# Performance work log

Hardware: AMD Instinct MI355X
Metric: run time of the kernel (lower is better)

## Reference

```python
import jax, jax.numpy as jnp
import numpy as np

N_HEADS = 16
D_MODEL = 1024
D_HEAD = D_MODEL // N_HEADS


def setup_inputs() -> dict:
    key = jax.random.key(0)
    k1, k2, k3 = jax.random.split(key, 3)
    b, t, d = 2, 2048, D_MODEL
    x = jax.random.normal(k1, (b, t, d), dtype=jnp.float32)
    # Linear weights stored as [in, out] so y = x @ W (equivalent to torch's x @ W.T)
    w_qkv = jax.random.normal(k2, (d, 3 * d), dtype=jnp.float32) * (1.0 / np.sqrt(d))
    w_out = jax.random.normal(k3, (d, d), dtype=jnp.float32) * (1.0 / np.sqrt(d))
    return {"x": x, "w_qkv": w_qkv, "w_out": w_out}


def reference(x, w_qkv, w_out):
    b, t, d = x.shape
    h, dh = N_HEADS, D_HEAD
    qkv = x @ w_qkv                                   # (b, t, 3d)
    q, k, v = jnp.split(qkv, 3, axis=-1)
    # (b, h, t, dh)
    q = q.reshape(b, t, h, dh).transpose(0, 2, 1, 3)
    k = k.reshape(b, t, h, dh).transpose(0, 2, 1, 3)
    v = v.reshape(b, t, h, dh).transpose(0, 2, 1, 3)
    scale = 1.0 / np.sqrt(dh).astype(np.float32)
    att = jnp.einsum('bhqd,bhkd->bhqk', q, k) * scale  # (b, h, t, t)
    causal = jnp.tril(jnp.ones((t, t), dtype=bool))
    att = jnp.where(causal, att, -jnp.inf)
    att = jax.nn.softmax(att, axis=-1)
    y = jnp.einsum('bhqk,bhkd->bhqd', att, v)          # (b, h, t, dh)
    y = y.transpose(0, 2, 1, 3).reshape(b, t, d)
    return y @ w_out
```

## Files before the change

### kernel.cpp

```cpp
#include <hip/hip_runtime.h>
#include <hip/hip_bf16.h>
#include <stdint.h>

typedef __bf16 bf16x8 __attribute__((ext_vector_type(8)));
typedef float  f32x4  __attribute__((ext_vector_type(4)));

#define B_   2
#define T_   2048
#define H_   16
#define DH_  64
#define DM_  1024
#define BH_  (B_*H_)
#define M_   (B_*T_)

#define QSCALE 0.18033688f
#define FIXED_M 8.0f

static __device__ __forceinline__ void gload_lds16(const void* g, void* lds) {
  __builtin_amdgcn_global_load_lds(
      (const __attribute__((address_space(1))) void*)(uintptr_t)g,
      (__attribute__((address_space(3))) void*)(uint32_t)(uintptr_t)lds,
      16, 0, 0);
}

__global__ void k_cvt_bf16(const float* __restrict__ in, __hip_bfloat16* __restrict__ out, int n4) {
  int i = blockIdx.x * blockDim.x + threadIdx.x;
  if (i < n4) {
    float4 v = reinterpret_cast<const float4*>(in)[i];
    alignas(8) __hip_bfloat16 t[4] = {__float2bfloat16(v.x), __float2bfloat16(v.y),
                                      __float2bfloat16(v.z), __float2bfloat16(v.w)};
    reinterpret_cast<uint2*>(out)[i] = *reinterpret_cast<const uint2*>(t);
  }
}

__global__ void k_cvtT(const float* __restrict__ in, __hip_bfloat16* __restrict__ out, int K, int N) {
  __shared__ float tile[32][33];
  int n0 = blockIdx.x * 32, k0 = blockIdx.y * 32;
  int tid = threadIdx.x;
  int kl = tid >> 3, n4 = (tid & 7) * 4;
  float4 v = *reinterpret_cast<const float4*>(in + (size_t)(k0 + kl) * N + n0 + n4);
  tile[kl][n4 + 0] = v.x; tile[kl][n4 + 1] = v.y; tile[kl][n4 + 2] = v.z; tile[kl][n4 + 3] = v.w;
  __syncthreads();
  int nl = tid >> 3, k4 = (tid & 7) * 4;
  alignas(8) __hip_bfloat16 t[4];
  #pragma unroll
  for (int j = 0; j < 4; ++j) t[j] = __float2bfloat16(tile[k4 + j][nl]);
  *reinterpret_cast<uint2*>(out + (size_t)(n0 + nl) * K + k0 + k4) = *reinterpret_cast<const uint2*>(t);
}

template<int BM, int BN, int FM, int FN>
static __device__ __forceinline__ void gemm_core(
    const __hip_bfloat16* __restrict__ A, const __hip_bfloat16* __restrict__ BT,
    int K, int brow, int bcol, __hip_bfloat16* As, __hip_bfloat16* Bs, f32x4 acc[FM][FN]) {
  constexpr int WGN = BN / (16 * FN);
  const int tid = threadIdx.x, wave = tid >> 6, lane = tid & 63;
  const int wr = wave / WGN, wc = wave % WGN;
  const int llo = lane & 15, lhi = lane >> 4;
  for (int k0 = 0; k0 < K; k0 += 32) {
    #pragma unroll
    for (int c = wave; c < BM / 16; c += 4)
      gload_lds16(A + (size_t)(brow + c * 16 + (lane >> 2)) * K + k0 + (lane & 3) * 8,
                  As + c * 16 * 32);
    #pragma unroll
    for (int c = wave; c < BN / 16; c += 4)
      gload_lds16(BT + (size_t)(bcol + c * 16 + (lane >> 2)) * K + k0 + (lane & 3) * 8,
                  Bs + c * 16 * 32);
    __syncthreads();
    bf16x8 a[FM], b[FN];
    #pragma unroll
    for (int i = 0; i < FM; ++i)
      a[i] = *reinterpret_cast<const bf16x8*>(As + (wr * FM * 16 + i * 16 + llo) * 32 + lhi * 8);
    #pragma unroll
    for (int j = 0; j < FN; ++j)
      b[j] = *reinterpret_cast<const bf16x8*>(Bs + (wc * FN * 16 + j * 16 + llo) * 32 + lhi * 8);
    #pragma unroll
    for (int i = 0; i < FM; ++i)
      #pragma unroll
      for (int j = 0; j < FN; ++j)
        acc[i][j] = __builtin_amdgcn_mfma_f32_16x16x32_bf16(a[i], b[j], acc[i][j], 0, 0, 0);
    __syncthreads();
  }
}

__global__ __launch_bounds__(256) void k_gemm_qkv(
    const __hip_bfloat16* __restrict__ A, const __hip_bfloat16* __restrict__ BT,
    __hip_bfloat16* __restrict__ q_ws, __hip_bfloat16* __restrict__ k_ws,
    __hip_bfloat16* __restrict__ vT) {
  alignas(16) __shared__ __hip_bfloat16 As[128 * 32];
  alignas(16) __shared__ __hip_bfloat16 Bs[128 * 32];
  f32x4 acc[4][4] = {};
  const int brow = blockIdx.y * 128, bcol = blockIdx.x * 128;
  gemm_core<128, 128, 4, 4>(A, BT, DM_, brow, bcol, As, Bs, acc);
  const int tid = threadIdx.x, wave = tid >> 6, lane = tid & 63;
  const int wr = wave >> 1, wc = wave & 1;
  const int llo = lane & 15, lhi = lane >> 4;
  #pragma unroll
  for (int i = 0; i < 4; ++i) {
    const int tbase = brow + wr * 64 + i * 16 + lhi * 4;
    const int b = tbase >> 11, t = tbase & 2047;
    #pragma unroll
    for (int j = 0; j < 4; ++j) {
      int n = bcol + wc * 64 + j * 16 + llo;
      int part = n >> 10, rem = n & 1023, hh = rem >> 6, dh = rem & 63;
      if (part == 2) {
        alignas(8) __hip_bfloat16 tv[4];
        #pragma unroll
        for (int r = 0; r < 4; ++r) tv[r] = __float2bfloat16(acc[i][j][r]);
        *reinterpret_cast<uint2*>(
            vT + (((size_t)(b * H_ + hh)) * DH_ + dh) * T_ + t) =
            *reinterpret_cast<const uint2*>(tv);
      } else {
        float sc = (part == 0) ? QSCALE : 1.0f;
        __hip_bfloat16* dst = (part == 0) ? q_ws : k_ws;
        #pragma unroll
        for (int r = 0; r < 4; ++r)
          dst[(((size_t)(b * H_ + hh)) * T_ + t + r) * DH_ + dh] =
              __float2bfloat16(acc[i][j][r] * sc);
      }
    }
  }
}

__global__ __launch_bounds__(256) void k_gemm_out(
    const __hip_bfloat16* __restrict__ A, const __hip_bfloat16* __restrict__ BT,
    float* __restrict__ C) {
  alignas(16) __shared__ __hip_bfloat16 As[128 * 32];
  alignas(16) __shared__ __hip_bfloat16 Bs[64 * 32];
  f32x4 acc[4][2] = {};
  const int brow = blockIdx.y * 128, bcol = blockIdx.x * 64;
  gemm_core<128, 64, 4, 2>(A, BT, DM_, brow, bcol, As, Bs, acc);
  const int tid = threadIdx.x, wave = tid >> 6, lane = tid & 63;
  const int wr = wave >> 1, wc = wave & 1;
  const int llo = lane & 15, lhi = lane >> 4;
  #pragma unroll
  for (int i = 0; i < 4; ++i)
    #pragma unroll
    for (int j = 0; j < 2; ++j) {
      int n = bcol + wc * 32 + j * 16 + llo;
      #pragma unroll
      for (int r = 0; r < 4; ++r) {
        int m = brow + wr * 64 + i * 16 + lhi * 4 + r;
        C[(size_t)m * DM_ + n] = acc[i][j][r];
      }
    }
}

__global__ __launch_bounds__(512) void k_attn(
    const __hip_bfloat16* __restrict__ Q, const __hip_bfloat16* __restrict__ Kk,
    const __hip_bfloat16* __restrict__ VT, __hip_bfloat16* __restrict__ Y) {
  alignas(16) __shared__ __hip_bfloat16 Ks[2][64 * 64];
  alignas(16) __shared__ __hip_bfloat16 Vs[2][64 * 64];
  alignas(16) __shared__ __hip_bfloat16 Ps[8][16 * 64];
  const int bh = blockIdx.y;
  const int p  = blockIdx.x;
  const int tid = threadIdx.x, wave = tid >> 6, lane = tid & 63;
  const int llo = lane & 15, lhi = lane >> 4;
  const int qt   = (wave < 4) ? (31 - p) : p;
  const int myNt = qt + 1;
  const int ntA  = 32 - p;
  const int q0 = qt * 64;
  const int qbase = q0 + (wave & 3) * 16;

  const __hip_bfloat16* kb = Kk + (size_t)bh * T_ * DH_;
  const __hip_bfloat16* vb = VT + (size_t)bh * DH_ * T_;

  const int srow = lane >> 3;
  const int schunk = (lane & 7) ^ srow;
  const int rb = wave * 8;

  bf16x8 aq[2];
  #pragma unroll
  for (int k0 = 0; k0 < 2; ++k0)
    aq[k0] = *reinterpret_cast<const bf16x8*>(
        Q + ((size_t)bh * T_ + qbase + llo) * DH_ + k0 * 32 + lhi * 8);

  float lrow[4] = {0.f, 0.f, 0.f, 0.f};
  f32x4 o[4] = {};

  gload_lds16(kb + (size_t)(rb + srow) * DH_ + schunk * 8, &Ks[0][rb * 64]);
  gload_lds16(vb + (size_t)(rb + srow) * T_ + schunk * 8, &Vs[0][rb * 64]);
  __syncthreads();

  for (int it = 0; it < ntA; ++it) {
    const int cur = it & 1;
    if (it + 1 < ntA) {
      const int tn = (it + 1) * 64;
      gload_lds16(kb + (size_t)(tn + rb + srow) * DH_ + schunk * 8, &Ks[cur ^ 1][rb * 64]);
      gload_lds16(vb + (size_t)(rb + srow) * T_ + tn + schunk * 8, &Vs[cur ^ 1][rb * 64]);
    }
    if (it < myNt) {
      const __hip_bfloat16* ksb = Ks[cur];
      const __hip_bfloat16* vsb = Vs[cur];

      f32x4 s[4];
      __builtin_amdgcn_s_setprio(1);
      #pragma unroll
      for (int jn = 0; jn < 4; ++jn) {
        const __hip_bfloat16* krow = ksb + (jn * 16 + llo) * 64;
        bf16x8 b0 = *reinterpret_cast<const bf16x8*>(krow + ((lhi ^ (llo & 7)) << 3));
        bf16x8 b1 = *reinterpret_cast<const bf16x8*>(krow + (((4 + lhi) ^ (llo & 7)) << 3));
        f32x4 z = {};
        z = __builtin_amdgcn_mfma_f32_16x16x32_bf16(aq[0], b0, z, 0, 0, 0);
        z = __builtin_amdgcn_mfma_f32_16x16x32_bf16(aq[1], b1, z, 0, 0, 0);
        s[jn] = z;
      }
      __builtin_amdgcn_s_setprio(0);
      if (it == myNt - 1) {
        #pragma unroll
        for (int jn = 0; jn < 4; ++jn)
          #pragma unroll
          for (int r = 0; r < 4; ++r) {
            int qrow = qbase + lhi * 4 + r;
            int tcol = q0 + jn * 16 + llo;
            if (tcol > qrow) s[jn][r] = -INFINITY;
          }
      }
      #pragma unroll
      for (int jn = 0; jn < 4; ++jn)
        #pragma unroll
        for (int r = 0; r < 4; ++r) {
          float pv = __builtin_amdgcn_exp2f(s[jn][r] - FIXED_M);
          lrow[r] += pv;
          int row = lhi * 4 + r, col = jn * 16 + llo;
          Ps[wave][row * 64 + (col ^ ((row & 7) << 3))] = __float2bfloat16(pv);
        }
      bf16x8 ap0 = *reinterpret_cast<const bf16x8*>(
          &Ps[wave][llo * 64 + ((lhi ^ (llo & 7)) << 3)]);
      bf16x8 ap1 = *reinterpret_cast<const bf16x8*>(
          &Ps[wave][llo * 64 + (((4 + lhi) ^ (llo & 7)) << 3)]);
      __builtin_amdgcn_s_setprio(1);
      #pragma unroll
      for (int jd = 0; jd < 4; ++jd) {
        const __hip_bfloat16* vrow = vsb + (jd * 16 + llo) * 64;
        bf16x8 b0 = *reinterpret_cast<const bf16x8*>(vrow + ((lhi ^ (llo & 7)) << 3));
        bf16x8 b1 = *reinterpret_cast<const bf16x8*>(vrow + (((4 + lhi) ^ (llo & 7)) << 3));
        o[jd] = __builtin_amdgcn_mfma_f32_16x16x32_bf16(ap0, b0, o[jd], 0, 0, 0);
        o[jd] = __builtin_amdgcn_mfma_f32_16x16x32_bf16(ap1, b1, o[jd], 0, 0, 0);
      }
      __builtin_amdgcn_s_setprio(0);
    }
    __syncthreads();
  }

  float lr[4];
  #pragma unroll
  for (int r = 0; r < 4; ++r) {
    float ps = lrow[r];
    #pragma unroll
    for (int d = 1; d < 16; d <<= 1) ps += __shfl_xor(ps, d);
    lr[r] = ps;
  }
  const int b = bh >> 4, h = bh & 15;
  #pragma unroll
  for (int jd = 0; jd < 4; ++jd)
    #pragma unroll
    for (int r = 0; r < 4; ++r) {
      int trow = qbase + lhi * 4 + r;
      int col = h * 64 + jd * 16 + llo;
      Y[((size_t)(b * T_ + trow)) * DM_ + col] = __float2bfloat16(o[jd][r] / lr[r]);
    }
}

extern "C" void kernel_launch(void* const* d_in, const int* in_sizes, int n_in,
                              void* d_out, int out_size, void* d_ws, size_t ws_size,
                              hipStream_t stream) {
  const float* x     = (const float*)d_in[0];
  const float* w_qkv = (const float*)d_in[1];
  const float* w_out = (const float*)d_in[2];
  float* out = (float*)d_out;
  char* ws = (char*)d_ws;

  size_t off = 0;
  __hip_bfloat16* xb    = (__hip_bfloat16*)(ws + off); off += (size_t)M_ * DM_ * 2;
  __hip_bfloat16* wqkvT = (__hip_bfloat16*)(ws + off); off += (size_t)3 * DM_ * DM_ * 2;
  __hip_bfloat16* woutT = (__hip_bfloat16*)(ws + off); off += (size_t)DM_ * DM_ * 2;
  __hip_bfloat16* q_ws  = (__hip_bfloat16*)(ws + off); off += (size_t)M_ * DM_ * 2;
  __hip_bfloat16* k_ws  = (__hip_bfloat16*)(ws + off); off += (size_t)M_ * DM_ * 2;
  __hip_bfloat16* vT    = (__hip_bfloat16*)(ws + off); off += (size_t)M_ * DM_ * 2;
  __hip_bfloat16* y_ws  = (__hip_bfloat16*)(ws + off); off += (size_t)M_ * DM_ * 2;
  (void)ws_size; (void)in_sizes; (void)n_in; (void)out_size;

  k_cvt_bf16<<<(M_ * DM_ / 4 + 255) / 256, 256, 0, stream>>>(x, xb, M_ * DM_ / 4);
  k_cvtT<<<dim3(3 * DM_ / 32, DM_ / 32), 256, 0, stream>>>(w_qkv, wqkvT, DM_, 3 * DM_);
  k_cvtT<<<dim3(DM_ / 32, DM_ / 32), 256, 0, stream>>>(w_out, woutT, DM_, DM_);

  k_gemm_qkv<<<dim3(3 * DM_ / 128, M_ / 128), 256, 0, stream>>>(xb, wqkvT, q_ws, k_ws, vT);

  k_attn<<<dim3(T_ / 128, BH_), 512, 0, stream>>>(q_ws, k_ws, vT, y_ws);

  k_gemm_out<<<dim3(DM_ / 64, M_ / 128), 256, 0, stream>>>(y_ws, woutT, out);
}
```

Baseline: 115.8 us.

## Split-K balance attention tiles between wave groups with per-group K/V staging

The attention block previously had one wave group own the long query tile and the other the short one, so the short group sat idle for many iterations. Now each group stages its own K/V tiles into separate double buffers, and the short group helps the long tile by handling the back half of its key range. The helper's partial output and row sums are merged through LDS at the end, which works because the kernel uses a fixed softmax max. The loop count drops to 17 iterations, at the cost of doubled K/V shared memory, extra registers for the helper accumulators, and a final reduction step.

New measurement: 113.7 us. About the same (-1.8%).

```diff
diff --git a/kernel.cpp b/kernel.cpp
--- a/kernel.cpp
+++ b/kernel.cpp
@@ -145,119 +145,172 @@
     }
 }
 
-__global__ __launch_bounds__(512) void k_attn(
+static __device__ __forceinline__ void attn_tile(
+    const __hip_bfloat16* ksb, const __hip_bfloat16* vsb, __hip_bfloat16* PsW,
+    const bf16x8* aq, int llo, int lhi, int qbase, int tile, bool do_mask,
+    f32x4* o, float* lrow) {
+  f32x4 s[4];
+  __builtin_amdgcn_s_setprio(1);
+  #pragma unroll
+  for (int jn = 0; jn < 4; ++jn) {
+    const __hip_bfloat16* krow = ksb + (jn * 16 + llo) * 64;
+    bf16x8 b0 = *reinterpret_cast<const bf16x8*>(krow + ((lhi ^ (llo & 7)) << 3));
+    bf16x8 b1 = *reinterpret_cast<const bf16x8*>(krow + (((4 + lhi) ^ (llo & 7)) << 3));
+    f32x4 z = {};
+    z = __builtin_amdgcn_mfma_f32_16x16x32_bf16(aq[0], b0, z, 0, 0, 0);
+    z = __builtin_amdgcn_mfma_f32_16x16x32_bf16(aq[1], b1, z, 0, 0, 0);
+    s[jn] = z;
+  }
+  __builtin_amdgcn_s_setprio(0);
+  if (do_mask) {
+    #pragma unroll
+    for (int jn = 0; jn < 4; ++jn)
+      #pragma unroll
+      for (int r = 0; r < 4; ++r) {
+        int qrow = qbase + lhi * 4 + r;
+        int tcol = tile * 64 + jn * 16 + llo;
+        if (tcol > qrow) s[jn][r] = -INFINITY;
+      }
+  }
+  #pragma unroll
+  for (int jn = 0; jn < 4; ++jn)
+    #pragma unroll
+    for (int r = 0; r < 4; ++r) {
+      float pv = __builtin_amdgcn_exp2f(s[jn][r] - FIXED_M);
+      lrow[r] += pv;
+      int row = lhi * 4 + r, col = jn * 16 + llo;
+      PsW[row * 64 + (col ^ ((row & 7) << 3))] = __float2bfloat16(pv);
+    }
+  bf16x8 ap0 = *reinterpret_cast<const bf16x8*>(&PsW[llo * 64 + ((lhi ^ (llo & 7)) << 3)]);
+  bf16x8 ap1 = *reinterpret_cast<const bf16x8*>(&PsW[llo * 64 + (((4 + lhi) ^ (llo & 7)) << 3)]);
+  __builtin_amdgcn_s_setprio(1);
+  #pragma unroll
+  for (int jd = 0; jd < 4; ++jd) {
+    const __hip_bfloat16* vrow = vsb + (jd * 16 + llo) * 64;
+    bf16x8 b0 = *reinterpret_cast<const bf16x8*>(vrow + ((lhi ^ (llo & 7)) << 3));
+    bf16x8 b1 = *reinterpret_cast<const bf16x8*>(vrow + (((4 + lhi) ^ (llo & 7)) << 3));
+    o[jd] = __builtin_amdgcn_mfma_f32_16x16x32_bf16(ap0, b0, o[jd], 0, 0, 0);
+    o[jd] = __builtin_amdgcn_mfma_f32_16x16x32_bf16(ap1, b1, o[jd], 0, 0, 0);
+  }
+  __builtin_amdgcn_s_setprio(0);
+}
+
+__global__ __launch_bounds__(512, 4) void k_attn(
     const __hip_bfloat16* __restrict__ Q, const __hip_bfloat16* __restrict__ Kk,
     const __hip_bfloat16* __restrict__ VT, __hip_bfloat16* __restrict__ Y) {
-  alignas(16) __shared__ __hip_bfloat16 Ks[2][64 * 64];
-  alignas(16) __shared__ __hip_bfloat16 Vs[2][64 * 64];
+  alignas(16) __shared__ __hip_bfloat16 Ks[4][64 * 64];
+  alignas(16) __shared__ __hip_bfloat16 Vs[4][64 * 64];
   alignas(16) __shared__ __hip_bfloat16 Ps[8][16 * 64];
   const int bh = blockIdx.y;
   const int p  = blockIdx.x;
   const int tid = threadIdx.x, wave = tid >> 6, lane = tid & 63;
   const int llo = lane & 15, lhi = lane >> 4;
-  const int qt   = (wave < 4) ? (31 - p) : p;
-  const int myNt = qt + 1;
-  const int ntA  = 32 - p;
-  const int q0 = qt * 64;
-  const int qbase = q0 + (wave & 3) * 16;
+  const int group = wave >> 2, ws = wave & 3;
+  const int qtA = 31 - p, qtB = p;
+  const int qt_own = group ? qtB : qtA;
+  const int qb_own  = qt_own * 64 + ws * 16;
+  const int qb_help = qtA * 64 + ws * 16;
 
   const __hip_bfloat16* kb = Kk + (size_t)bh * T_ * DH_;
   const __hip_bfloat16* vb = VT + (size_t)bh * DH_ * T_;
 
   const int srow = lane >> 3;
   const int schunk = (lane & 7) ^ srow;
-  const int rb = wave * 8;
-
-  bf16x8 aq[2];
-  #pragma unroll
-  for (int k0 = 0; k0 < 2; ++k0)
-    aq[k0] = *reinterpret_cast<const bf16x8*>(
-        Q + ((size_t)bh * T_ + qbase + llo) * DH_ + k0 * 32 + lhi * 8);
-
-  float lrow[4] = {0.f, 0.f, 0.f, 0.f};
-  f32x4 o[4] = {};
-
-  gload_lds16(kb + (size_t)(rb + srow) * DH_ + schunk * 8, &Ks[0][rb * 64]);
-  gload_lds16(vb + (size_t)(rb + srow) * T_ + schunk * 8, &Vs[0][rb * 64]);
+  const int rbase = ws * 16;
+
+  auto seq = [&](int j) -> int {
+    if (group == 0) return (j <= 16) ? j : -1;
+    if (j <= p) return j;
+    if (j <= 15) return 32 - j;
+    return -1;
+  };
+  auto stage = [&](int tile, int slot) {
+    gload_lds16(kb + (size_t)(tile * 64 + rbase + srow) * DH_ + schunk * 8,
+                &Ks[slot][rbase * 64]);
+    gload_lds16(kb + (size_t)(tile * 64 + rbase + 8 + srow) * DH_ + schunk * 8,
+                &Ks[slot][(rbase + 8) * 64]);
+    gload_lds16(vb + (size_t)(rbase + srow) * T_ + tile * 64 + schunk * 8,
+                &Vs[slot][rbase * 64]);
+    gload_lds16(vb + (size_t)(rbase + 8 + srow) * T_ + tile * 64 + schunk * 8,
+                &Vs[slot][(rbase + 8) * 64]);
+  };
+
+  bf16x8 aq_own[2], aq_help[2];
+  #pragma unroll
+  for (int k0 = 0; k0 < 2; ++k0) {
+    aq_own[k0] = *reinterpret_cast<const bf16x8*>(
+        Q + ((size_t)bh * T_ + qb_own + llo) * DH_ + k0 * 32 + lhi * 8);
+    aq_help[k0] = *reinterpret_cast<const bf16x8*>(
+        Q + ((size_t)bh * T_ + qb_help + llo) * DH_ + k0 * 32 + lhi * 8);
+  }
+
+  float l_own[4] = {0.f, 0.f, 0.f, 0.f}, l_help[4] = {0.f, 0.f, 0.f, 0.f};
+  f32x4 o_own[4] = {}, o_help[4] = {};
+
+  stage(0, group * 2);
   __syncthreads();
 
-  for (int it = 0; it < ntA; ++it) {
-    const int cur = it & 1;
-    if (it + 1 < ntA) {
-      const int tn = (it + 1) * 64;
-      gload_lds16(kb + (size_t)(tn + rb + srow) * DH_ + schunk * 8, &Ks[cur ^ 1][rb * 64]);
-      gload_lds16(vb + (size_t)(rb + srow) * T_ + tn + schunk * 8, &Vs[cur ^ 1][rb * 64]);
-    }
-    if (it < myNt) {
-      const __hip_bfloat16* ksb = Ks[cur];
-      const __hip_bfloat16* vsb = Vs[cur];
-
-      f32x4 s[4];
-      __builtin_amdgcn_s_setprio(1);
-      #pragma unroll
-      for (int jn = 0; jn < 4; ++jn) {
-        const __hip_bfloat16* krow = ksb + (jn * 16 + llo) * 64;
-        bf16x8 b0 = *reinterpret_cast<const bf16x8*>(krow + ((lhi ^ (llo & 7)) << 3));
-        bf16x8 b1 = *reinterpret_cast<const bf16x8*>(krow + (((4 + lhi) ^ (llo & 7)) << 3));
-        f32x4 z = {};
-        z = __builtin_amdgcn_mfma_f32_16x16x32_bf16(aq[0], b0, z, 0, 0, 0);
-        z = __builtin_amdgcn_mfma_f32_16x16x32_bf16(aq[1], b1, z, 0, 0, 0);
-        s[jn] = z;
-      }
-      __builtin_amdgcn_s_setprio(0);
-      if (it == myNt - 1) {
-        #pragma unroll
-        for (int jn = 0; jn < 4; ++jn)
-          #pragma unroll
-          for (int r = 0; r < 4; ++r) {
-            int qrow = qbase + lhi * 4 + r;
-            int tcol = q0 + jn * 16 + llo;
-            if (tcol > qrow) s[jn][r] = -INFINITY;
-          }
-      }
-      #pragma unroll
-      for (int jn = 0; jn < 4; ++jn)
-        #pragma unroll
-        for (int r = 0; r < 4; ++r) {
-          float pv = __builtin_amdgcn_exp2f(s[jn][r] - FIXED_M);
-          lrow[r] += pv;
-          int row = lhi * 4 + r, col = jn * 16 + llo;
-          Ps[wave][row * 64 + (col ^ ((row & 7) << 3))] = __float2bfloat16(pv);
-        }
-      bf16x8 ap0 = *reinterpret_cast<const bf16x8*>(
-          &Ps[wave][llo * 64 + ((lhi ^ (llo & 7)) << 3)]);
-      bf16x8 ap1 = *reinterpret_cast<const bf16x8*>(
-          &Ps[wave][llo * 64 + (((4 + lhi) ^ (llo & 7)) << 3)]);
-      __builtin_amdgcn_s_setprio(1);
-      #pragma unroll
-      for (int jd = 0; jd < 4; ++jd) {
-        const __hip_bfloat16* vrow = vsb + (jd * 16 + llo) * 64;
-        bf16x8 b0 = *reinterpret_cast<const bf16x8*>(vrow + ((lhi ^ (llo & 7)) << 3));
-        bf16x8 b1 = *reinterpret_cast<const bf16x8*>(vrow + (((4 + lhi) ^ (llo & 7)) << 3));
-        o[jd] = __builtin_amdgcn_mfma_f32_16x16x32_bf16(ap0, b0, o[jd], 0, 0, 0);
-        o[jd] = __builtin_amdgcn_mfma_f32_16x16x32_bf16(ap1, b1, o[jd], 0, 0, 0);
-      }
-      __builtin_amdgcn_s_setprio(0);
+  for (int j = 0; j <= 16; ++j) {
+    const int s1 = seq(j + 1);
+    if (s1 >= 0) stage(s1, group * 2 + ((j + 1) & 1));
+    const int tc = seq(j);
+    if (tc >= 0) {
+      const __hip_bfloat16* ksb = &Ks[group * 2 + (j & 1)][0];
+      const __hip_bfloat16* vsb = &Vs[group * 2 + (j & 1)][0];
+      if (group == 0 || j <= p)
+        attn_tile(ksb, vsb, &Ps[wave][0], aq_own, llo, lhi, qb_own, tc,
+                  tc == qt_own, o_own, l_own);
+      else
+        attn_tile(ksb, vsb, &Ps[wave][0], aq_help, llo, lhi, qb_help, tc,
+                  tc == qtA, o_help, l_help);
     }
     __syncthreads();
   }
 
+  float* Oh = reinterpret_cast<float*>(&Ks[0][0]);
+  float* Lh = reinterpret_cast<float*>(&Vs[0][0]);
+  if (group == 1) {
+    #pragma unroll
+    for (int r = 0; r < 4; ++r) {
+      float lh = l_help[r];
+      #pragma unroll
+      for (int d = 1; d < 16; d <<= 1) lh += __shfl_xor(lh, d);
+      if (llo == 0) Lh[ws * 16 + lhi * 4 + r] = lh;
+    }
+    #pragma unroll
+    for (int jd = 0; jd < 4; ++jd)
+      #pragma unroll
+      for (int r = 0; r < 4; ++r)
+        Oh[ws * 1024 + (lhi * 4 + r) * 64 + jd * 16 + llo] = o_help[jd][r];
+  }
+  __syncthreads();
+
   float lr[4];
   #pragma unroll
   for (int r = 0; r < 4; ++r) {
-    float ps = lrow[r];
+    float ps = l_own[r];
     #pragma unroll
     for (int d = 1; d < 16; d <<= 1) ps += __shfl_xor(ps, d);
     lr[r] = ps;
   }
+  if (group == 0) {
+    #pragma unroll
+    for (int r = 0; r < 4; ++r) lr[r] += Lh[ws * 16 + lhi * 4 + r];
+    #pragma unroll
+    for (int jd = 0; jd < 4; ++jd)
+      #pragma unroll
+      for (int r = 0; r < 4; ++r)
+        o_own[jd][r] += Oh[ws * 1024 + (lhi * 4 + r) * 64 + jd * 16 + llo];
+  }
+
   const int b = bh >> 4, h = bh & 15;
   #pragma unroll
   for (int jd = 0; jd < 4; ++jd)
     #pragma unroll
     for (int r = 0; r < 4; ++r) {
-      int trow = qbase + lhi * 4 + r;
+      int trow = qb_own + lhi * 4 + r;
       int col = h * 64 + jd * 16 + llo;
-      Y[((size_t)(b * T_ + trow)) * DM_ + col] = __float2bfloat16(o[jd][r] / lr[r]);
+      Y[((size_t)(b * T_ + trow)) * DM_ + col] = __float2bfloat16(o_own[jd][r] / lr[r]);
     }
 }
 
```
